# Kernel tuning notes

Hardware: AMD Instinct MI355X
Metric: run time of the kernel (lower is better)

The kernel has to match this reference:

```python
import jax, jax.numpy as jnp
import numpy as np

S, T, C, L_GNN, L_TF, H = 8, 16, 128, 3, 2, 4
B = 512
FF = 4 * C
EPS = 1e-5


def setup_inputs() -> dict:
    key = jax.random.key(0)
    ks = jax.random.split(key, 24)
    w = lambda k, shape: jax.random.normal(k, shape, jnp.float32) * 0.05
    inp = {}
    inp["xx"] = jax.random.randint(ks[0], (B, T, S, S, S), 0, 3, dtype=jnp.int32)
    inp["ss"] = jax.random.uniform(ks[1], (B, 1), jnp.float32)
    # DynamicGNNv2 params
    inp["Win"] = w(ks[2], (C, 5)); inp["b_in"] = w(ks[3], (C,))
    inp["Wl"] = w(ks[4], (L_GNN, C, C)); inp["bl"] = w(ks[5], (L_GNN, C))   # SAGEConv lin_l (neighbors)
    inp["Wr"] = w(ks[6], (L_GNN, C, C))                                      # SAGEConv lin_r (root, no bias)
    inp["ln_g"] = jnp.ones((C,), jnp.float32); inp["ln_b"] = jnp.zeros((C,), jnp.float32)  # shared LayerNorm
    # TransformerEncoder params (norm_first, relu, dropout=0 at eval)
    inp["Wqkv"] = w(ks[7], (L_TF, 3 * C, C)); inp["bqkv"] = w(ks[8], (L_TF, 3 * C))
    inp["Wo"] = w(ks[9], (L_TF, C, C)); inp["bo"] = w(ks[10], (L_TF, C))
    inp["ln1_g"] = jnp.ones((L_TF, C), jnp.float32); inp["ln1_b"] = jnp.zeros((L_TF, C), jnp.float32)
    inp["ln2_g"] = jnp.ones((L_TF, C), jnp.float32); inp["ln2_b"] = jnp.zeros((L_TF, C), jnp.float32)
    inp["W1"] = w(ks[11], (L_TF, FF, C)); inp["b1"] = w(ks[12], (L_TF, FF))
    inp["W2"] = w(ks[13], (L_TF, C, FF)); inp["b2"] = w(ks[14], (L_TF, C))
    inp["Wact"] = w(ks[15], (C, S ** 3)); inp["bact"] = w(ks[16], (C,))
    inp["Wsc"] = w(ks[17], (C, 1)); inp["bsc"] = w(ks[18], (C,))
    return inp


def layernorm(x, g, b):
    mu = x.mean(-1, keepdims=True)
    var = ((x - mu) ** 2).mean(-1, keepdims=True)
    return (x - mu) * jax.lax.rsqrt(var + EPS) * g + b


def reference(xx, ss, Win, b_in, Wl, bl, Wr, ln_g, ln_b, Wqkv, bqkv, Wo, bo,
              ln1_g, ln1_b, ln2_g, ln2_b, W1, b1, W2, b2, Wact, bact, Wsc, bsc):
    Bc = xx.shape[0]
    S3 = S ** 3
    frame0 = xx[:, 0].reshape(Bc, S3).astype(jnp.float32)            # (B,S^3)
    m = (frame0 != 0).astype(jnp.float32)                            # active-node mask
    grid = jnp.arange(S3)
    i, j, k = grid // (S * S), (grid // S) % S, grid % S
    coord = jnp.stack([i, j, k], -1).astype(jnp.float32) / (S - 1)   # (S^3,3)
    feat = jnp.concatenate([
        jnp.broadcast_to(coord, (Bc, S3, 3)),
        (frame0 / 2.0)[..., None],
        jnp.broadcast_to((ss / S)[:, None, :], (Bc, S3, 1)),
    ], -1)                                                            # (B,S^3,5)
    x = feat @ Win.T + b_in                                           # lin_in
    mm = m[..., None]
    n = m.sum(-1, keepdims=True)[..., None]                           # nodes per graph (B,1,1)
    for l in range(L_GNN):
        # complete graph (no self loops): mean over neighbors = (sum_active - self)/(N-1)
        s = (x * mm).sum(1, keepdims=True)                            # (B,1,C)
        neigh = jnp.where(n > 1, (s - x) / jnp.maximum(n - 1.0, 1.0), 0.0)
        h = neigh @ Wl[l].T + bl[l] + x @ Wr[l].T                     # SAGEConv
        x = layernorm(jax.nn.relu(h), ln_g, ln_b)
    full = x * mm                                                     # scatter-fill into dense (B,S^3,C)
    # pooling matmul: mean over each i/j/k slice -> (B,3S,C)
    poolW = jnp.concatenate([
        (i[None, :] == jnp.arange(S)[:, None]).astype(jnp.float32),
        (j[None, :] == jnp.arange(S)[:, None]).astype(jnp.float32),
        (k[None, :] == jnp.arange(S)[:, None]).astype(jnp.float32),
    ], 0)                                                             # (3S,S^3)
    gnn_emb = jnp.einsum('ps,bsc->bpc', poolW, full) / poolW.sum(1)[None, :, None]
    # transformer over past actions
    a = xx[:, 1:].reshape(Bc, T - 1, S3).astype(jnp.float32) @ Wact.T + bact
    Hd = C // H
    scale = 1.0 / np.sqrt(Hd).astype(np.float32)
    split_heads = lambda t: t.reshape(Bc, -1, H, Hd).transpose(0, 2, 1, 3)
    for l in range(L_TF):
        h1 = layernorm(a, ln1_g[l], ln1_b[l])
        q, kk, v = jnp.split(h1 @ Wqkv[l].T + bqkv[l], 3, axis=-1)
        q, kk, v = split_heads(q), split_heads(kk), split_heads(v)
        att = jax.nn.softmax(jnp.einsum('bhqd,bhkd->bhqk', q, kk) * scale, -1)
        o = jnp.einsum('bhqk,bhkd->bhqd', att, v).transpose(0, 2, 1, 3).reshape(Bc, -1, C)
        a = a + (o @ Wo[l].T + bo[l])
        h2 = layernorm(a, ln2_g[l], ln2_b[l])
        a = a + (jax.nn.relu(h2 @ W1[l].T + b1[l]) @ W2[l].T + b2[l])
    act_emb = a.mean(1)                                               # (B,C)
    mv_emb = jax.nn.relu(ss @ Wsc.T + bsc)                            # (B,C)
    return jnp.concatenate([gnn_emb, act_emb[:, None], mv_emb[:, None]], 1)  # (B,3S+2,C)
```

## Files before the change

kernel.cpp:

```cpp
#include <hip/hip_runtime.h>
#include <hip/hip_bf16.h>
#include <string.h>

typedef __hip_bfloat16 bf16;
typedef __attribute__((ext_vector_type(8))) short short8;
typedef __attribute__((ext_vector_type(4))) float f32x4;

#define Bsz 512
#define S3  512
#define Tsz 16
#define Cc  128
#define TT  15
#define EPSv 1e-5f

__device__ __forceinline__ float u2f(unsigned short u) {
    return __uint_as_float(((unsigned)u) << 16);
}
__device__ __forceinline__ float ulo(unsigned u) { return __uint_as_float(u << 16); }
__device__ __forceinline__ float uhi(unsigned u) { return __uint_as_float(u & 0xffff0000u); }
__device__ __forceinline__ unsigned short f2bu(float v) {
    bf16 h = __float2bfloat16(v);
    unsigned short u; memcpy(&u, &h, 2); return u;
}
__device__ __forceinline__ unsigned short bfr16(float a) {
    unsigned u = __float_as_uint(a);
    u = u + 0x7fffu + ((u >> 16) & 1u);
    return (unsigned short)(u >> 16);
}
__device__ __forceinline__ unsigned fpack2(float a, float b) {
    unsigned ua = __float_as_uint(a), ub = __float_as_uint(b);
    ua = ua + 0x7fffu + ((ua >> 16) & 1u);
    ub = ub + 0x7fffu + ((ub >> 16) & 1u);
    return (ua >> 16) | (ub & 0xffff0000u);
}
__device__ __forceinline__ float dot4(float4 a, float4 b) {
    return a.x*b.x + a.y*b.y + a.z*b.z + a.w*b.w;
}

__global__ __launch_bounds__(256) void k_tpack(const float* __restrict__ src,
                                               float* __restrict__ dst,
                                               int NR, int NK)
{
    __shared__ float tile[32][33];
    int k0 = blockIdx.x * 32, r0 = blockIdx.y * 32;
    int lr = threadIdx.x >> 5, lk = threadIdx.x & 31;
    for (int i = lr; i < 32; i += 8)
        tile[i][lk] = src[(size_t)(r0 + i) * NK + k0 + lk];
    __syncthreads();
    int c = threadIdx.x & 31, k4 = threadIdx.x >> 5;
    float4 v;
    v.x = tile[c][k4 * 4 + 0]; v.y = tile[c][k4 * 4 + 1];
    v.z = tile[c][k4 * 4 + 2]; v.w = tile[c][k4 * 4 + 3];
    ((float4*)dst)[(size_t)(k0 / 4 + k4) * NR + r0 + c] = v;
}

__global__ __launch_bounds__(256) void k_cvt5(
    const float* __restrict__ s0, const float* __restrict__ s1,
    const float* __restrict__ s2, const float* __restrict__ s3,
    const float* __restrict__ s4, ushort* __restrict__ dst)
{
    int i = blockIdx.x * 256 + threadIdx.x;
    if (i >= 114688) return;
    const float* src; int rel;
    if (i < 16384)      { src = s0; rel = i; }
    else if (i < 40960) { src = s1; rel = i - 16384; }
    else if (i < 49152) { src = s2; rel = i - 40960; }
    else if (i < 81920) { src = s3; rel = i - 49152; }
    else                { src = s4; rel = i - 81920; }
    float4 v = ((const float4*)src)[rel];
    ushort4 o;
    o.x = f2bu(v.x); o.y = f2bu(v.y); o.z = f2bu(v.z); o.w = f2bu(v.w);
    ((ushort4*)dst)[i] = o;
}

__global__ __launch_bounds__(256) void k_wpack(
    const float* __restrict__ Wl, const float* __restrict__ Wr,
    ushort* __restrict__ WB)
{
    int l = blockIdx.x, w = blockIdx.y;
    const float* src = (w == 0 ? Wl : Wr) + l * 16384;
    ushort* dst = WB + (size_t)(l * 2 + w) * 32 * 512;
    for (int item = threadIdx.x; item < 2048; item += 256) {
        int f = item >> 6, lane = item & 63;
        int t = f >> 2, ks = f & 3, ml = lane & 15, q = lane >> 4;
        int n = t * 16 + ml, kb = ks * 32 + q * 8;
        const float4* sp = (const float4*)(src + n * 128 + kb);
        float4 v0 = sp[0], v1 = sp[1];
        ushort4 o0, o1;
        o0.x = f2bu(v0.x); o0.y = f2bu(v0.y); o0.z = f2bu(v0.z); o0.w = f2bu(v0.w);
        o1.x = f2bu(v1.x); o1.y = f2bu(v1.y); o1.z = f2bu(v1.z); o1.w = f2bu(v1.w);
        ushort* dp = dst + (size_t)f * 512 + lane * 8;
        *(ushort4*)dp = o0;
        *(ushort4*)(dp + 4) = o1;
    }
}

__global__ __launch_bounds__(512, 2) void k_torso(
    const int* __restrict__ xx, const float* __restrict__ ss,
    const float* __restrict__ Win, const float* __restrict__ b_in,
    const ushort* __restrict__ WB,
    const float4* __restrict__ WlP, const float* __restrict__ blv,
    const float* __restrict__ lng, const float* __restrict__ lnb,
    float* __restrict__ out)
{
    __shared__ ushort X[512 * 136];
    __shared__ float  mC[512];
    __shared__ float  sred[8 * 128];
    __shared__ float  ssc[128];
    __shared__ float  sbase[128];
    __shared__ float  gln[128], bln[128];
    __shared__ float  scnt[8];
    __shared__ float  invS;

    int b = blockIdx.x, tid = threadIdx.x;
    int wv = tid >> 6, lane = tid & 63;
    int ml = lane & 15, quad = lane >> 4;

    {
        int cp = lane;
        int co0 = 2 * cp, co1 = 2 * cp + 1;
        const int* x0 = xx + (size_t)b * Tsz * S3;
        float f4c = ss[b] * (1.0f / 8.0f);
        float a0 = Win[co0*5+0], a1 = Win[co0*5+1], a2 = Win[co0*5+2], a3 = Win[co0*5+3];
        float c0 = Win[co1*5+0], c1 = Win[co1*5+1], c2 = Win[co1*5+2], c3 = Win[co1*5+3];
        float ba = b_in[co0] + f4c * Win[co0*5+4];
        float bc = b_in[co1] + f4c * Win[co1*5+4];
        float sp0 = 0.f, sp1 = 0.f; int cnt = 0;
        for (int node = wv; node < S3; node += 8) {
            int f0 = x0[node];
            float m = (f0 != 0) ? 1.f : 0.f;
            float ci = (float)(node >> 6) * (1.f / 7.f);
            float cj = (float)((node >> 3) & 7) * (1.f / 7.f);
            float ck = (float)(node & 7) * (1.f / 7.f);
            float ft = (float)f0 * 0.5f;
            float v0 = ba + ci * a0 + cj * a1 + ck * a2 + ft * a3;
            float v1 = bc + ci * c0 + cj * c1 + ck * c2 + ft * c3;
            ((unsigned*)(X + node * 136))[cp] = fpack2(v0, v1);
            sp0 += v0 * m; sp1 += v1 * m;
            cnt += (f0 != 0);
            if (cp == 0) mC[node] = m;
        }
        sred[wv * 128 + co0] = sp0;
        sred[wv * 128 + co1] = sp1;
        if (cp == 0) scnt[wv] = (float)cnt;
    }
    if (tid < 128) { gln[tid] = lng[tid]; bln[tid] = lnb[tid]; }
    __syncthreads();
    if (tid == 0) {
        float n = 0.f;
#pragma unroll
        for (int g = 0; g < 8; g++) n += scnt[g];
        invS = (n > 1.f) ? 1.f / (n - 1.f) : 0.f;
    }
    __syncthreads();
    if (tid < 128) {
        float s = 0.f;
#pragma unroll
        for (int g = 0; g < 8; g++) s += sred[g * 128 + tid];
        ssc[tid] = s * invS;
    }
    __syncthreads();
    if (tid < 128) {
        float a = blv[tid];
        for (int k4 = 0; k4 < 32; k4++)
            a += dot4(*(const float4*)(ssc + k4 * 4), WlP[k4 * 384 + tid]);
        sbase[tid] = a;
    }
    __syncthreads();

    float ninv = -invS;

    for (int l = 0; l < 3; l++) {
        bool last = (l == 2);
        float sp[8];
#pragma unroll
        for (int t = 0; t < 8; t++) sp[t] = 0.f;

        f32x4 acc[8][4];
#pragma unroll
        for (int t = 0; t < 8; t++)
#pragma unroll
            for (int mm = 0; mm < 4; mm++) acc[t][mm] = (f32x4){0.f, 0.f, 0.f, 0.f};

        const ushort* xrb = X + (wv * 64 + ml) * 136 + quad * 8;

#pragma unroll 1
        for (int pass = 0; pass < 2; pass++) {
            const ushort* wp = WB + ((size_t)(l * 2 + pass) * 32) * 512 + lane * 8;
#pragma unroll
            for (int ks = 0; ks < 4; ks++) {
                short8 a[4];
#pragma unroll
                for (int mm = 0; mm < 4; mm++)
                    a[mm] = *(const short8*)(xrb + mm * 16 * 136 + ks * 32);
#pragma unroll
                for (int t = 0; t < 8; t++) {
                    short8 bg = *(const short8*)(wp + (size_t)(t * 4 + ks) * 512);
#pragma unroll
                    for (int mm = 0; mm < 4; mm++)
                        acc[t][mm] = __builtin_amdgcn_mfma_f32_16x16x32_bf16(a[mm], bg, acc[t][mm], 0, 0, 0);
                }
            }
            if (pass == 0) {
#pragma unroll
                for (int t = 0; t < 8; t++)
#pragma unroll
                    for (int mm = 0; mm < 4; mm++)
#pragma unroll
                        for (int r = 0; r < 4; r++)
                            acc[t][mm][r] *= ninv;
            }
        }

        float bse[8], gg[8], be[8];
#pragma unroll
        for (int t = 0; t < 8; t++) {
            bse[t] = sbase[t * 16 + ml];
            gg[t]  = gln[t * 16 + ml];
            be[t]  = bln[t * 16 + ml];
        }
#pragma unroll
        for (int mm = 0; mm < 4; mm++) {
#pragma unroll
            for (int r = 0; r < 4; r++) {
                int row = wv * 64 + mm * 16 + quad * 4 + r;
                float s = 0.f, q = 0.f;
#pragma unroll
                for (int t = 0; t < 8; t++) {
                    float v = fmaxf(acc[t][mm][r] + bse[t], 0.f);
                    acc[t][mm][r] = v;
                    s += v; q += v * v;
                }
#pragma unroll
                for (int off = 1; off <= 8; off <<= 1) {
                    s += __shfl_xor(s, off, 64);
                    q += __shfl_xor(q, off, 64);
                }
                float mu = s * (1.f / 128.f);
                float rs = rsqrtf(q * (1.f / 128.f) - mu * mu + EPSv);
                float mrow = mC[row];
#pragma unroll
                for (int t = 0; t < 8; t++) {
                    float y = (acc[t][mm][r] - mu) * rs * gg[t] + be[t];
                    if (last) y *= mrow;
                    else sp[t] += y * mrow;
                    X[row * 136 + t * 16 + ml] = bfr16(y);
                }
            }
        }

        if (!last) {
#pragma unroll
            for (int t = 0; t < 8; t++) {
                sp[t] += __shfl_xor(sp[t], 16, 64);
                sp[t] += __shfl_xor(sp[t], 32, 64);
            }
            if (quad == 0) {
#pragma unroll
                for (int t = 0; t < 8; t++) sred[wv * 128 + t * 16 + ml] = sp[t];
            }
            __syncthreads();
            if (tid < 128) {
                float s = 0.f;
#pragma unroll
                for (int g = 0; g < 8; g++) s += sred[g * 128 + tid];
                ssc[tid] = s * invS;
            }
            __syncthreads();
            if (tid < 128) {
                float a = blv[(l + 1) * 128 + tid];
                for (int k4 = 0; k4 < 32; k4++)
                    a += dot4(*(const float4*)(ssc + k4 * 4), WlP[k4 * 384 + (l + 1) * 128 + tid]);
                sbase[tid] = a;
            }
            __syncthreads();
        }
    }
    __syncthreads();

    for (int item = tid; item < 768; item += 512) {
        int c4 = item & 31, p = item >> 5;
        int axis = p >> 3, idx = p & 7;
        float4 sum = {0.f, 0.f, 0.f, 0.f};
        for (int t = 0; t < 64; t++) {
            int node;
            if (axis == 0)      node = idx * 64 + t;
            else if (axis == 1) node = (t >> 3) * 64 + idx * 8 + (t & 7);
            else                node = t * 8 + idx;
            uint2 pk = *(const uint2*)(X + node * 136 + c4 * 4);
            sum.x += ulo(pk.x);
            sum.y += uhi(pk.x);
            sum.z += ulo(pk.y);
            sum.w += uhi(pk.y);
        }
        float4 o;
        o.x = sum.x * (1.f / 64.f); o.y = sum.y * (1.f / 64.f);
        o.z = sum.z * (1.f / 64.f); o.w = sum.w * (1.f / 64.f);
        *(float4*)(out + (size_t)b * 26 * Cc + p * Cc + c4 * 4) = o;
    }
}

__global__ __launch_bounds__(256) void k_tf3(
    const int* __restrict__ xx, const float* __restrict__ ss,
    const ushort* __restrict__ WactB, const float* __restrict__ bact,
    const ushort* __restrict__ WqkvB, const float* __restrict__ bqkv,
    const ushort* __restrict__ WoB, const float* __restrict__ bo,
    const float* __restrict__ ln1g, const float* __restrict__ ln1b,
    const float* __restrict__ ln2g, const float* __restrict__ ln2b,
    const ushort* __restrict__ W1B, const float* __restrict__ b1v,
    const ushort* __restrict__ W2B, const float* __restrict__ b2v,
    const float* __restrict__ Wsc, const float* __restrict__ bsc,
    float* __restrict__ out)
{
    __shared__ float  As[TT * 132];
    __shared__ ushort Qs[16 * 392];
    __shared__ ushort Ab[16 * 136];
    __shared__ ushort Hs[16 * 136];
    __shared__ ushort Fs[16 * 520];
    __shared__ float  Att[60 * 16];
    __shared__ float  mu_s[TT], rs_s[TT];

    int b = blockIdx.x, tid = threadIdx.x;
    int wv = tid >> 6, lane = tid & 63;
    int ml = lane & 15, quad = lane >> 4;

    const int* xa = xx + (size_t)b * Tsz * S3 + S3;
    for (int f = tid; f < TT * 512; f += 256) {
        int t = f >> 9, s = f & 511;
        Fs[t * 520 + s] = bfr16((float)xa[t * 512 + s]);
    }
    __syncthreads();

    {
        f32x4 acc[2];
#pragma unroll
        for (int i = 0; i < 2; i++) acc[i] = (f32x4){0.f, 0.f, 0.f, 0.f};
        const ushort* ar = Fs + ml * 520 + quad * 8;
        for (int ks = 0; ks < 16; ks++) {
            short8 a = *(const short8*)(ar + ks * 32);
#pragma unroll
            for (int i = 0; i < 2; i++) {
                int n0 = (wv * 2 + i) * 16;
                short8 bfr = *(const short8*)(WactB + (size_t)(n0 + ml) * 512 + quad * 8 + ks * 32);
                acc[i] = __builtin_amdgcn_mfma_f32_16x16x32_bf16(a, bfr, acc[i], 0, 0, 0);
            }
        }
#pragma unroll
        for (int i = 0; i < 2; i++) {
            int col = (wv * 2 + i) * 16 + ml;
            float bb = bact[col];
#pragma unroll
            for (int r = 0; r < 4; r++) {
                int row = quad * 4 + r;
                if (row < TT) As[row * 132 + col] = acc[i][r] + bb;
            }
        }
    }
    __syncthreads();

    for (int l = 0; l < 2; l++) {
        const float* bq  = bqkv + l * 384;
        const float* bol = bo + l * 128;
        const float* g1  = ln1g + l * 128; const float* be1 = ln1b + l * 128;
        const float* g2  = ln2g + l * 128; const float* be2 = ln2b + l * 128;
        const float* b1l = b1v + l * 512;  const float* b2l = b2v + l * 128;

        for (int r = wv; r < TT; r += 4) {
            float2 v = *(const float2*)(As + r * 132 + lane * 2);
            float s = v.x + v.y, q = v.x * v.x + v.y * v.y;
            for (int off = 32; off; off >>= 1) {
                s += __shfl_xor(s, off, 64);
                q += __shfl_xor(q, off, 64);
            }
            if (lane == 0) {
                float mu = s * (1.f / 128.f);
                mu_s[r] = mu;
                rs_s[r] = rsqrtf(q * (1.f / 128.f) - mu * mu + EPSv);
            }
        }
        __syncthreads();
        for (int f = tid; f < TT * 64; f += 256) {
            int t = f >> 6, cp = f & 63;
            float mu = mu_s[t], rs = rs_s[t];
            float x0 = (As[t * 132 + 2 * cp]     - mu) * rs * g1[2 * cp]     + be1[2 * cp];
            float x1 = (As[t * 132 + 2 * cp + 1] - mu) * rs * g1[2 * cp + 1] + be1[2 * cp + 1];
            ((unsigned*)(Ab + t * 136))[cp] = fpack2(x0, x1);
        }
        __syncthreads();

        {
            short8 a[4];
            const ushort* ar = Ab + ml * 136 + quad * 8;
#pragma unroll
            for (int ks = 0; ks < 4; ks++) a[ks] = *(const short8*)(ar + ks * 32);
#pragma unroll
            for (int i = 0; i < 6; i++) {
                int n0 = (wv * 6 + i) * 16;
                f32x4 acc = (f32x4){0.f, 0.f, 0.f, 0.f};
                const ushort* wb = WqkvB + (size_t)(l * 384 + n0 + ml) * 128 + quad * 8;
#pragma unroll
                for (int ks = 0; ks < 4; ks++) {
                    short8 bfr = *(const short8*)(wb + ks * 32);
                    acc = __builtin_amdgcn_mfma_f32_16x16x32_bf16(a[ks], bfr, acc, 0, 0, 0);
                }
                int col = n0 + ml;
                float bb = bq[col];
#pragma unroll
                for (int r = 0; r < 4; r++) {
                    int row = quad * 4 + r;
                    if (row < TT) Qs[row * 392 + col] = bfr16(acc[r] + bb);
                }
            }
        }
        __syncthreads();

        if (tid < 60) {
            int h = tid / 15, tq = tid % 15;
            const ushort* qp = Qs + tq * 392 + h * 32;
            float sc[TT];
            float mx = -1e30f;
#pragma unroll
            for (int tk = 0; tk < TT; tk++) {
                const ushort* kp = Qs + tk * 392 + 128 + h * 32;
                float d = 0.f;
#pragma unroll
                for (int u = 0; u < 32; u += 4) {
                    uint2 qa = *(const uint2*)(qp + u);
                    uint2 ka = *(const uint2*)(kp + u);
                    d += ulo(qa.x) * ulo(ka.x) + uhi(qa.x) * uhi(ka.x)
                       + ulo(qa.y) * ulo(ka.y) + uhi(qa.y) * uhi(ka.y);
                }
                d *= 0.17677669529663689f;
                sc[tk] = d; mx = fmaxf(mx, d);
            }
            float sum = 0.f;
#pragma unroll
            for (int tk = 0; tk < TT; tk++) { float e = __expf(sc[tk] - mx); sc[tk] = e; sum += e; }
            float r = 1.f / sum;
#pragma unroll
            for (int tk = 0; tk < TT; tk++) Att[tid * 16 + tk] = sc[tk] * r;
        }
        __syncthreads();

        for (int f = tid; f < TT * 64; f += 256) {
            int t = f >> 6, cp = f & 63;
            int h = cp >> 4;
            const float* ap = Att + (h * 15 + t) * 16;
            const ushort* vp = Qs + 256 + 2 * cp;
            float a0 = 0.f, a1 = 0.f;
#pragma unroll
            for (int tk = 0; tk < TT; tk++) {
                float w = ap[tk];
                unsigned pk = *(const unsigned*)(vp + tk * 392);
                a0 += w * ulo(pk);
                a1 += w * uhi(pk);
            }
            ((unsigned*)(Hs + t * 136))[cp] = fpack2(a0, a1);
        }
        __syncthreads();

        {
            short8 a[4];
            const ushort* ar = Hs + ml * 136 + quad * 8;
#pragma unroll
            for (int ks = 0; ks < 4; ks++) a[ks] = *(const short8*)(ar + ks * 32);
#pragma unroll
            for (int i = 0; i < 2; i++) {
                int n0 = (wv * 2 + i) * 16;
                f32x4 acc = (f32x4){0.f, 0.f, 0.f, 0.f};
                const ushort* wb = WoB + (size_t)(l * 128 + n0 + ml) * 128 + quad * 8;
#pragma unroll
                for (int ks = 0; ks < 4; ks++) {
                    short8 bfr = *(const short8*)(wb + ks * 32);
                    acc = __builtin_amdgcn_mfma_f32_16x16x32_bf16(a[ks], bfr, acc, 0, 0, 0);
                }
                int col = n0 + ml;
                float bb = bol[col];
#pragma unroll
                for (int r = 0; r < 4; r++) {
                    int row = quad * 4 + r;
                    if (row < TT) As[row * 132 + col] += acc[r] + bb;
                }
            }
        }
        __syncthreads();

        for (int r = wv; r < TT; r += 4) {
            float2 v = *(const float2*)(As + r * 132 + lane * 2);
            float s = v.x + v.y, q = v.x * v.x + v.y * v.y;
            for (int off = 32; off; off >>= 1) {
                s += __shfl_xor(s, off, 64);
                q += __shfl_xor(q, off, 64);
            }
            if (lane == 0) {
                float mu = s * (1.f / 128.f);
                mu_s[r] = mu;
                rs_s[r] = rsqrtf(q * (1.f / 128.f) - mu * mu + EPSv);
            }
        }
        __syncthreads();
        for (int f = tid; f < TT * 64; f += 256) {
            int t = f >> 6, cp = f & 63;
            float mu = mu_s[t], rs = rs_s[t];
            float x0 = (As[t * 132 + 2 * cp]     - mu) * rs * g2[2 * cp]     + be2[2 * cp];
            float x1 = (As[t * 132 + 2 * cp + 1] - mu) * rs * g2[2 * cp + 1] + be2[2 * cp + 1];
            ((unsigned*)(Ab + t * 136))[cp] = fpack2(x0, x1);
        }
        __syncthreads();

        {
            short8 a[4];
            const ushort* ar = Ab + ml * 136 + quad * 8;
#pragma unroll
            for (int ks = 0; ks < 4; ks++) a[ks] = *(const short8*)(ar + ks * 32);
#pragma unroll
            for (int i = 0; i < 8; i++) {
                int n0 = (wv * 8 + i) * 16;
                f32x4 acc = (f32x4){0.f, 0.f, 0.f, 0.f};
                const ushort* wb = W1B + (size_t)(l * 512 + n0 + ml) * 128 + quad * 8;
#pragma unroll
                for (int ks = 0; ks < 4; ks++) {
                    short8 bfr = *(const short8*)(wb + ks * 32);
                    acc = __builtin_amdgcn_mfma_f32_16x16x32_bf16(a[ks], bfr, acc, 0, 0, 0);
                }
                int col = n0 + ml;
                float bb = b1l[col];
#pragma unroll
                for (int r = 0; r < 4; r++) {
                    int row = quad * 4 + r;
                    if (row < TT) Fs[row * 520 + col] = bfr16(fmaxf(acc[r] + bb, 0.f));
                }
            }
        }
        __syncthreads();

        {
            f32x4 acc[2];
#pragma unroll
            for (int i = 0; i < 2; i++) acc[i] = (f32x4){0.f, 0.f, 0.f, 0.f};
            const ushort* ar = Fs + ml * 520 + quad * 8;
            for (int ks = 0; ks < 16; ks++) {
                short8 a = *(const short8*)(ar + ks * 32);
#pragma unroll
                for (int i = 0; i < 2; i++) {
                    int n0 = (wv * 2 + i) * 16;
                    short8 bfr = *(const short8*)(W2B + (size_t)(l * 128 + n0 + ml) * 512 + quad * 8 + ks * 32);
                    acc[i] = __builtin_amdgcn_mfma_f32_16x16x32_bf16(a, bfr, acc[i], 0, 0, 0);
                }
            }
#pragma unroll
            for (int i = 0; i < 2; i++) {
                int col = (wv * 2 + i) * 16 + ml;
                float bb = b2l[col];
#pragma unroll
                for (int r = 0; r < 4; r++) {
                    int row = quad * 4 + r;
                    if (row < TT) As[row * 132 + col] += acc[i][r] + bb;
                }
            }
        }
        __syncthreads();
    }

    if (tid < 128) {
        float s = 0.f;
#pragma unroll
        for (int t = 0; t < TT; t++) s += As[t * 132 + tid];
        out[(size_t)b * 26 * Cc + 24 * Cc + tid] = s * (1.f / 15.f);
    } else if (tid < 256) {
        int co = tid - 128;
        float v = ss[b] * Wsc[co] + bsc[co];
        out[(size_t)b * 26 * Cc + 25 * Cc + co] = fmaxf(v, 0.f);
    }
}

extern "C" void kernel_launch(void* const* d_in, const int* in_sizes, int n_in,
                              void* d_out, int out_size, void* d_ws, size_t ws_size,
                              hipStream_t stream)
{
    (void)in_sizes; (void)n_in; (void)out_size; (void)ws_size;
    const int*   xx   = (const int*)d_in[0];
    const float* ss   = (const float*)d_in[1];
    const float* Win  = (const float*)d_in[2];
    const float* b_in = (const float*)d_in[3];
    const float* Wl   = (const float*)d_in[4];
    const float* bl   = (const float*)d_in[5];
    const float* Wr   = (const float*)d_in[6];
    const float* lng  = (const float*)d_in[7];
    const float* lnb  = (const float*)d_in[8];
    const float* Wqkv = (const float*)d_in[9];
    const float* bqkv = (const float*)d_in[10];
    const float* Wo   = (const float*)d_in[11];
    const float* bo   = (const float*)d_in[12];
    const float* ln1g = (const float*)d_in[13];
    const float* ln1b = (const float*)d_in[14];
    const float* ln2g = (const float*)d_in[15];
    const float* ln2b = (const float*)d_in[16];
    const float* W1   = (const float*)d_in[17];
    const float* b1   = (const float*)d_in[18];
    const float* W2   = (const float*)d_in[19];
    const float* b2   = (const float*)d_in[20];
    const float* Wact = (const float*)d_in[21];
    const float* bact = (const float*)d_in[22];
    const float* Wsc  = (const float*)d_in[23];
    const float* bsc  = (const float*)d_in[24];
    float* out = (float*)d_out;

    char* ws = (char*)d_ws;
    size_t off = 0;
    float* WlT  = (float*)(ws + off); off += 384 * 128 * 4;
    ushort* WB    = (ushort*)(ws + off); off += (size_t)3 * 2 * 128 * 128 * 2;
    ushort* WactB = (ushort*)(ws + off); off += 128 * 512 * 2;
    ushort* WqkvB = (ushort*)(ws + off); off += 768 * 128 * 2;
    ushort* WoB   = (ushort*)(ws + off); off += 256 * 128 * 2;
    ushort* W1B   = (ushort*)(ws + off); off += 1024 * 128 * 2;
    ushort* W2B   = (ushort*)(ws + off); off += 256 * 512 * 2;

    k_tpack<<<dim3(4, 12), 256, 0, stream>>>(Wl, WlT, 384, 128);
    k_cvt5<<<448, 256, 0, stream>>>(Wact, Wqkv, Wo, W1, W2, WactB);
    k_wpack<<<dim3(3, 2), 256, 0, stream>>>(Wl, Wr, WB);

    k_torso<<<Bsz, 512, 0, stream>>>(xx, ss, Win, b_in, WB,
                                     (const float4*)WlT, bl, lng, lnb, out);

    k_tf3<<<Bsz, 256, 0, stream>>>(xx, ss,
                                   WactB, bact, WqkvB, bqkv, WoB, bo,
                                   ln1g, ln1b, ln2g, ln2b,
                                   W1B, b1, W2B, b2,
                                   Wsc, bsc, out);
}
```

Before: 336.1 us.

## Interleave torso channel layout so LayerNorm epilogue writes packed bf16 pairs

Changes the channel ordering of the torso's shared activation buffer so that each lane's two MFMA output tiles (t and t+16 channels) sit adjacent. This lets the LayerNorm epilogue write 32-bit packed bf16 pairs instead of 16-bit scalar stores. The weight packing, initial feature write and pooled output store are all permuted to match. It also swaps the manual bf16 rounding for the hardware v_cvt_pk_bf16_f32 instruction and splits the epilogue into separate last and not-last branches. The added cost is more scattered float2 global stores in the pooling output.

```diff
diff --git a/kernel.cpp b/kernel.cpp
--- a/kernel.cpp
+++ b/kernel.cpp
@@ -28,14 +28,14 @@
     return (unsigned short)(u >> 16);
 }
 __device__ __forceinline__ unsigned fpack2(float a, float b) {
-    unsigned ua = __float_as_uint(a), ub = __float_as_uint(b);
-    ua = ua + 0x7fffu + ((ua >> 16) & 1u);
-    ub = ub + 0x7fffu + ((ub >> 16) & 1u);
-    return (ua >> 16) | (ub & 0xffff0000u);
+    unsigned r;
+    asm("v_cvt_pk_bf16_f32 %0, %1, %2" : "=v"(r) : "v"(a), "v"(b));
+    return r;
 }
 __device__ __forceinline__ float dot4(float4 a, float4 b) {
     return a.x*b.x + a.y*b.y + a.z*b.z + a.w*b.w;
 }
+
 
 __global__ __launch_bounds__(256) void k_tpack(const float* __restrict__ src,
                                                float* __restrict__ dst,
@@ -83,12 +83,14 @@
     for (int item = threadIdx.x; item < 2048; item += 256) {
         int f = item >> 6, lane = item & 63;
         int t = f >> 2, ks = f & 3, ml = lane & 15, q = lane >> 4;
-        int n = t * 16 + ml, kb = ks * 32 + q * 8;
-        const float4* sp = (const float4*)(src + n * 128 + kb);
-        float4 v0 = sp[0], v1 = sp[1];
+        int n = t * 16 + ml;
+        const float* sA = src + n * 128 + 32 * ks + q * 4;
+        const float* sB = sA + 16;
+        float4 a = *(const float4*)sA;
+        float4 b = *(const float4*)sB;
         ushort4 o0, o1;
-        o0.x = f2bu(v0.x); o0.y = f2bu(v0.y); o0.z = f2bu(v0.z); o0.w = f2bu(v0.w);
-        o1.x = f2bu(v1.x); o1.y = f2bu(v1.y); o1.z = f2bu(v1.z); o1.w = f2bu(v1.w);
+        o0.x = f2bu(a.x); o0.y = f2bu(b.x); o0.z = f2bu(a.y); o0.w = f2bu(b.y);
+        o1.x = f2bu(a.z); o1.y = f2bu(b.z); o1.z = f2bu(a.w); o1.w = f2bu(b.w);
         ushort* dp = dst + (size_t)f * 512 + lane * 8;
         *(ushort4*)dp = o0;
         *(ushort4*)(dp + 4) = o1;
@@ -118,7 +120,7 @@
 
     {
         int cp = lane;
-        int co0 = 2 * cp, co1 = 2 * cp + 1;
+        int co0 = 32 * (cp >> 4) + (cp & 15), co1 = co0 + 16;
         const int* x0 = xx + (size_t)b * Tsz * S3;
         float f4c = ss[b] * (1.0f / 8.0f);
         float a0 = Win[co0*5+0], a1 = Win[co0*5+1], a2 = Win[co0*5+2], a3 = Win[co0*5+3];
@@ -224,12 +226,13 @@
 #pragma unroll
             for (int r = 0; r < 4; r++) {
                 int row = wv * 64 + mm * 16 + quad * 4 + r;
+                float v[8];
                 float s = 0.f, q = 0.f;
 #pragma unroll
                 for (int t = 0; t < 8; t++) {
-                    float v = fmaxf(acc[t][mm][r] + bse[t], 0.f);
-                    acc[t][mm][r] = v;
-                    s += v; q += v * v;
+                    float vv = fmaxf(acc[t][mm][r] + bse[t], 0.f);
+                    v[t] = vv;
+                    s += vv; q = fmaf(vv, vv, q);
                 }
 #pragma unroll
                 for (int off = 1; off <= 8; off <<= 1) {
@@ -239,12 +242,23 @@
                 float mu = s * (1.f / 128.f);
                 float rs = rsqrtf(q * (1.f / 128.f) - mu * mu + EPSv);
                 float mrow = mC[row];
-#pragma unroll
-                for (int t = 0; t < 8; t++) {
-                    float y = (acc[t][mm][r] - mu) * rs * gg[t] + be[t];
-                    if (last) y *= mrow;
-                    else sp[t] += y * mrow;
-                    X[row * 136 + t * 16 + ml] = bfr16(y);
+                unsigned* xr32 = (unsigned*)(X + row * 136);
+                if (last) {
+#pragma unroll
+                    for (int t2 = 0; t2 < 4; t2++) {
+                        float y0 = ((v[2*t2]   - mu) * rs * gg[2*t2]   + be[2*t2])   * mrow;
+                        float y1 = ((v[2*t2+1] - mu) * rs * gg[2*t2+1] + be[2*t2+1]) * mrow;
+                        xr32[t2 * 16 + ml] = fpack2(y0, y1);
+                    }
+                } else {
+#pragma unroll
+                    for (int t2 = 0; t2 < 4; t2++) {
+                        float y0 = (v[2*t2]   - mu) * rs * gg[2*t2]   + be[2*t2];
+                        float y1 = (v[2*t2+1] - mu) * rs * gg[2*t2+1] + be[2*t2+1];
+                        sp[2*t2]   = fmaf(y0, mrow, sp[2*t2]);
+                        sp[2*t2+1] = fmaf(y1, mrow, sp[2*t2+1]);
+                        xr32[t2 * 16 + ml] = fpack2(y0, y1);
+                    }
                 }
             }
         }
@@ -293,10 +307,12 @@
             sum.z += ulo(pk.y);
             sum.w += uhi(pk.y);
         }
-        float4 o;
-        o.x = sum.x * (1.f / 64.f); o.y = sum.y * (1.f / 64.f);
-        o.z = sum.z * (1.f / 64.f); o.w = sum.w * (1.f / 64.f);
-        *(float4*)(out + (size_t)b * 26 * Cc + p * Cc + c4 * 4) = o;
+        int E0 = 32 * (c4 >> 3) + 2 * (c4 & 7);
+        float* ob = out + (size_t)b * 26 * Cc + p * Cc;
+        float2 lo = {sum.x * (1.f / 64.f), sum.z * (1.f / 64.f)};
+        float2 hi = {sum.y * (1.f / 64.f), sum.w * (1.f / 64.f)};
+        *(float2*)(ob + E0)      = lo;
+        *(float2*)(ob + E0 + 16) = hi;
     }
 }
 
```

After: 338.0 us. Within noise of the previous version (+0.6%).
